# Kernel optimization log

Measured on AMD Instinct MI355X. Metric: run time of the kernel, lower is better.

The kernel has to match this reference:

```python
import jax, jax.numpy as jnp
import numpy as np

# Interpretation constants (external PersistentHomology class unavailable):
# each sample's feature vector is a point cloud of N_POINTS points in R^POINT_DIM.
N_POINTS = 1024
POINT_DIM = 128
WEIGHT = 1.0
N_TARGET_DIMS = 2  # target_dimensions = [0, 1]; H1 diagram is empty -> contributes 0


def _h0_mean_persistence(pts):
    """Exact H0 persistence of the Vietoris-Rips filtration of a point cloud.

    H0 pairs are (birth=0, death=w_e) for each edge w_e of the Euclidean MST,
    so persistence values are exactly the MST edge lengths (Prim's algorithm,
    vectorized over points, sequential over the N-1 tree-growth steps).
    pts: [N, d] -> scalar mean persistence.
    """
    n = pts.shape[0]
    mindist0 = jnp.linalg.norm(pts - pts[0], axis=-1)          # [N]
    visited0 = jnp.zeros((n,), dtype=bool).at[0].set(True)

    def step(carry, _):
        mindist, visited = carry
        masked = jnp.where(visited, jnp.inf, mindist)          # [N]
        j = jnp.argmin(masked)
        death = masked[j]                                      # MST edge length
        visited = visited.at[j].set(True)
        newd = jnp.linalg.norm(pts - pts[j], axis=-1)          # [N]
        mindist = jnp.minimum(mindist, newd)
        return (mindist, visited), death

    (_, _), deaths = jax.lax.scan(step, (mindist0, visited0), None, length=n - 1)
    return jnp.mean(deaths)


def setup_inputs() -> dict:
    key = jax.random.key(0)
    representations = jax.random.normal(key, (128, N_POINTS * POINT_DIM), dtype=jnp.float32)
    return {"representations": representations}


def reference(representations) -> jnp.ndarray:
    b = representations.shape[0]
    pts = representations.reshape(b, N_POINTS, POINT_DIM)      # per-sample point cloud
    per_sample = jax.vmap(_h0_mean_persistence)(pts)           # [B] mean H0 persistence
    # original: sum over batch and target dims (H1 empty), / (B * n_dims), * weight
    loss = jnp.sum(per_sample) / (b * N_TARGET_DIMS)
    return WEIGHT * loss
```

## Files before the change

kernel.cpp:

```cpp
#include <hip/hip_runtime.h>

typedef unsigned int uint_t;
typedef unsigned short ushort_t;
typedef unsigned char uchar_t;
typedef _Float16 h2 __attribute__((ext_vector_type(2)));
typedef _Float16 f16x8 __attribute__((ext_vector_type(8)));
typedef float f32x4 __attribute__((ext_vector_type(4)));

#define NPTS 1024
#define DIM  128
#define NH2  64

__device__ __forceinline__ float dot2f(uint_t a, uint_t b, float c) {
#if __has_builtin(__builtin_amdgcn_fdot2)
    return __builtin_amdgcn_fdot2(__builtin_bit_cast(h2, a),
                                  __builtin_bit_cast(h2, b), c, false);
#else
    h2 ha = __builtin_bit_cast(h2, a);
    h2 hb = __builtin_bit_cast(h2, b);
    c += (float)ha[0] * (float)hb[0];
    c += (float)ha[1] * (float)hb[1];
    return c;
#endif
}

__device__ __forceinline__ uint_t umin_u(uint_t a, uint_t b) { return a < b ? a : b; }
__device__ __forceinline__ uint_t umax_u(uint_t a, uint_t b) { return a > b ? a : b; }
__device__ __forceinline__ uint_t pk_min_u16(uint_t a, uint_t b) {
    uint_t d; asm("v_pk_min_u16 %0, %1, %2" : "=v"(d) : "v"(a), "v"(b)); return d;
}
__device__ __forceinline__ uint_t pk_max_u16(uint_t a, uint_t b) {
    uint_t d; asm("v_pk_max_u16 %0, %1, %2" : "=v"(d) : "v"(a), "v"(b)); return d;
}
__device__ __forceinline__ uint_t pk_sub_u16w(uint_t a, uint_t b) {
    uint_t d; asm("v_pk_sub_u16 %0, %1, %2" : "=v"(d) : "v"(a), "v"(b)); return d;
}

#define DPP_UMIN(x, ctrl)                                                       \
    x = umin_u(x, (uint_t)__builtin_amdgcn_update_dpp((int)(x), (int)(x),       \
                                                      (ctrl), 0xf, 0xf, false))
#define DPP_REDUCE(x)                                                           \
    do { DPP_UMIN(x, 0x111); DPP_UMIN(x, 0x112); DPP_UMIN(x, 0x114);            \
         DPP_UMIN(x, 0x118); DPP_UMIN(x, 0x142); DPP_UMIN(x, 0x143); } while (0)

#define SEL_LO 0x05020400u
#define SEL_HI 0x07020600u

__device__ __forceinline__ void gload16(const void* g, void* l) {
#if __has_builtin(__builtin_amdgcn_global_load_lds)
    __builtin_amdgcn_global_load_lds(
        (__attribute__((address_space(1))) void*)(g),
        (__attribute__((address_space(3))) void*)(l), 16, 0, 0);
#else
    *(uint4*)l = *(const uint4*)g;
#endif
}

__global__ __launch_bounds__(256)
void prep_kernel(const float* __restrict__ reps, ushort_t* __restrict__ P16,
                 float* __restrict__ norms) {
    const int t   = threadIdx.x;
    const int row = blockIdx.x * 16 + (t >> 4);
    const int kx  = (t & 15) * 8;
    const float* src = reps + (size_t)row * DIM + kx;
    float4 v0 = *(const float4*)src;
    float4 v1 = *(const float4*)(src + 4);
    _Float16 h[8] = {(_Float16)v0.x, (_Float16)v0.y, (_Float16)v0.z, (_Float16)v0.w,
                     (_Float16)v1.x, (_Float16)v1.y, (_Float16)v1.z, (_Float16)v1.w};
    float nrm = 0.f;
    uint_t pk[4];
#pragma unroll
    for (int i = 0; i < 4; ++i) {
        float a = (float)h[2 * i], b = (float)h[2 * i + 1];
        nrm += a * a + b * b;
        pk[i] = (uint_t)__builtin_bit_cast(ushort_t, h[2 * i]) |
                ((uint_t)__builtin_bit_cast(ushort_t, h[2 * i + 1]) << 16);
    }
    *(uint4*)(P16 + (size_t)row * DIM + kx) = make_uint4(pk[0], pk[1], pk[2], pk[3]);
#pragma unroll
    for (int m = 1; m <= 8; m <<= 1) nrm += __shfl_xor(nrm, m, 16);
    if ((t & 15) == 0) norms[row] = nrm;
}

__global__ __launch_bounds__(256)
void norms_kernel(const float* __restrict__ reps, float* __restrict__ norms) {
    const int t   = threadIdx.x;
    const int row = blockIdx.x * 16 + (t >> 4);
    const int kx  = (t & 15) * 8;
    const float* src = reps + (size_t)row * DIM + kx;
    float4 v0 = *(const float4*)src;
    float4 v1 = *(const float4*)(src + 4);
    float nrm = 0.f;
    {
        _Float16 h[8] = {(_Float16)v0.x, (_Float16)v0.y, (_Float16)v0.z, (_Float16)v0.w,
                         (_Float16)v1.x, (_Float16)v1.y, (_Float16)v1.z, (_Float16)v1.w};
#pragma unroll
        for (int i = 0; i < 8; ++i) { float a = (float)h[i]; nrm += a * a; }
    }
#pragma unroll
    for (int m = 1; m <= 8; m <<= 1) nrm += __shfl_xor(nrm, m, 16);
    if ((t & 15) == 0) norms[row] = nrm;
}

__device__ __forceinline__ int swz(int row, int seg) {
    return (row << 7) + (((seg ^ row) & 15) << 3);
}
__device__ __forceinline__ uint_t packh2(float a, float b) {
    h2 p; p[0] = (_Float16)a; p[1] = (_Float16)b;
    return __builtin_bit_cast(uint_t, p);
}

__device__ __forceinline__ void gram_core_epilogue(
        f32x4 acc[2][8], const float* nrmS, uchar_t* Ds,
        int ti, int tj, int lane, int w) {
    const int cj = lane & 15;
    const int r4 = (lane >> 4) * 4;
    float na[2][4], nb[8];
#pragma unroll
    for (int mt = 0; mt < 2; ++mt)
#pragma unroll
        for (int r = 0; r < 4; ++r)
            na[mt][r] = nrmS[ti * 128 + w * 32 + mt * 16 + r4 + r];
#pragma unroll
    for (int nt = 0; nt < 8; ++nt) nb[nt] = nrmS[tj * 128 + nt * 16 + cj];
#pragma unroll
    for (int mt = 0; mt < 2; ++mt)
#pragma unroll
        for (int nt = 0; nt < 8; ++nt) {
            const int gj = tj * 128 + nt * 16 + cj;
#pragma unroll
            for (int r = 0; r < 4; ++r) {
                const int gi = ti * 128 + w * 32 + mt * 16 + r4 + r;
                float d2 = fmaxf(na[mt][r] + nb[nt] - 2.f * acc[mt][nt][r], 0.f);
                uint_t q = (uint_t)(d2 * 0.5f + 0.5f);
                q = q > 255u ? 255u : q;
                Ds[((size_t)gi << 10) + gj] = (uchar_t)q;
            }
        }
}

__device__ __forceinline__ void stageB(const ushort_t* Ps, int tj,
                                       ushort_t* Bq, int t) {
#pragma unroll
    for (int i = 0; i < 8; ++i) {
        const int c   = t + i * 256;
        const int row = c >> 4;
        const int seg = (c ^ row) & 15;
        gload16(Ps + (((size_t)(tj * 128 + row)) << 7) + (size_t)seg * 8,
                Bq + (size_t)c * 8);
    }
}

__global__ __launch_bounds__(256, 2)
void gram16f_kernel(const ushort_t* __restrict__ P16, const float* __restrict__ norms,
                    uchar_t* __restrict__ D8, uint_t* __restrict__ NN4,
                    int xcd_affine) {
    __shared__ ushort_t Bt[2][128 * 128];
    __shared__ uchar_t  Ot[128 * 128];
    const int bid = blockIdx.x;
    int s, ti;
    if (xcd_affine) {
        const int x = bid & 7, k = bid >> 3;
        s  = x + ((k >> 3) << 3);
        ti = k & 7;
    } else {
        s  = bid >> 3;
        ti = bid & 7;
    }
    const int t = threadIdx.x, lane = t & 63, w = t >> 6;

    const ushort_t* Ps = P16 + ((size_t)s * NPTS << 7);
    const ushort_t* Pa = Ps + ((size_t)ti * 128 << 7);
    const float*  nrmS = norms + (size_t)s * NPTS;
    uchar_t*      Ds   = D8 + ((size_t)s << 20);

    const int mrow = lane & 15;
    const int lg   = lane >> 4;
    const int cj   = lane & 15;
    const int r4   = (lane >> 4) * 4;
    const uint_t rr  = (uint_t)(lane & 3);
    const uint_t cl4 = (uint_t)(lane & 12);

    float ha[2][4];
#pragma unroll
    for (int mt = 0; mt < 2; ++mt)
#pragma unroll
        for (int r = 0; r < 4; ++r)
            ha[mt][r] = 0.5f * nrmS[ti * 128 + w * 32 + mt * 16 + r4 + r] + 0.5f;

    const ushort_t* parow0 = Pa + ((w * 32 + mrow) << 7);
    const ushort_t* parow1 = Pa + ((w * 32 + 16 + mrow) << 7);

    uint_t nnr[2][4] = {{~0u, ~0u, ~0u, ~0u}, {~0u, ~0u, ~0u, ~0u}};

    const uint_t sel01 = rr | ((rr + 4u) << 8);

    stageB(Ps, 0, &Bt[0][0], t);
    __syncthreads();

    for (int tj = 0; tj < 8; ++tj) {
        ushort_t* Bq = &Bt[tj & 1][0];
        if (tj < 7) stageB(Ps, tj + 1, &Bt[(tj + 1) & 1][0], t);

        f32x4 acc[2][8] = {};
        f16x8 a0 = *(const f16x8*)(parow0 + lg * 8);
        f16x8 a1 = *(const f16x8*)(parow1 + lg * 8);
#pragma unroll
        for (int q = 0; q < 4; ++q) {
            const int seg = q * 4 + lg;
            f16x8 a0c = a0, a1c = a1;
            if (q < 3) {
                a0 = *(const f16x8*)(parow0 + ((q + 1) * 4 + lg) * 8);
                a1 = *(const f16x8*)(parow1 + ((q + 1) * 4 + lg) * 8);
            }
#pragma unroll
            for (int nt = 0; nt < 8; ++nt) {
                f16x8 b = *(const f16x8*)&Bq[swz(nt * 16 + mrow, seg)];
                acc[0][nt] = __builtin_amdgcn_mfma_f32_16x16x32_f16(a0c, b, acc[0][nt], 0, 0, 0);
                acc[1][nt] = __builtin_amdgcn_mfma_f32_16x16x32_f16(a1c, b, acc[1][nt], 0, 0, 0);
            }
        }

        float hb[8];
#pragma unroll
        for (int nt = 0; nt < 8; ++nt) hb[nt] = 0.5f * nrmS[tj * 128 + nt * 16 + cj];
        uint_t res[2][8];
#pragma unroll
        for (int mt = 0; mt < 2; ++mt)
#pragma unroll
            for (int nt = 0; nt < 8; ++nt) {
                uint_t cp = 0;
#pragma unroll
                for (int r = 0; r < 4; ++r) {
                    float f = (ha[mt][r] + hb[nt]) - acc[mt][nt][r];
#if __has_builtin(__builtin_amdgcn_cvt_pk_u8_f32)
                    cp = __builtin_amdgcn_cvt_pk_u8_f32(f, (uint_t)r, cp);
#else
                    uint_t qb = (uint_t)fminf(fmaxf(f, 0.f), 255.f);
                    cp |= qb << (8 * r);
#endif
                }
                uint_t d0 = (uint_t)__builtin_amdgcn_update_dpp((int)cp, (int)cp, 0x00, 0xf, 0xf, false);
                uint_t d1 = (uint_t)__builtin_amdgcn_update_dpp((int)cp, (int)cp, 0x55, 0xf, 0xf, false);
                uint_t d2 = (uint_t)__builtin_amdgcn_update_dpp((int)cp, (int)cp, 0xaa, 0xf, 0xf, false);
                uint_t d3 = (uint_t)__builtin_amdgcn_update_dpp((int)cp, (int)cp, 0xff, 0xf, 0xf, false);
                uint_t lo  = __builtin_amdgcn_perm(d1, d0, sel01);
                uint_t hi  = __builtin_amdgcn_perm(d3, d2, sel01);
                res[mt][nt] = __builtin_amdgcn_perm(hi, lo, 0x05040100u);
            }

        __syncthreads();
        const int lrb = w * 32 + r4 + (int)rr;
        const int c4b = lane & 12;
#pragma unroll
        for (int mt = 0; mt < 2; ++mt)
#pragma unroll
            for (int nt = 0; nt < 8; ++nt) {
                const int lr = lrb + mt * 16;
                const int cs = nt ^ (lr & 7);
                *(uint_t*)&Ot[lr * 128 + cs * 16 + c4b] = res[mt][nt];
            }
        __syncthreads();
        {
            const int r8 = lane >> 3, c = lane & 7;
#pragma unroll
            for (int k = 0; k < 4; ++k) {
                const int row = w * 32 + k * 8 + r8;
                const int cs  = c ^ (row & 7);
                uint4 vv = *(const uint4*)&Ot[row * 128 + cs * 16];
                *(uint4*)(Ds + (((size_t)(ti * 128 + row)) << 10) + tj * 128 + c * 16) = vv;
            }
        }

#pragma unroll
        for (int mt = 0; mt < 2; ++mt) {
            uint_t md[16];
#pragma unroll
            for (int nt = 0; nt < 8; ++nt) {
                const uint_t base = (uint_t)(nt * 16) + cl4;
                md[2 * nt]     = __builtin_amdgcn_perm(res[mt][nt],
                                     ((base + 1u) << 16) | base, SEL_LO);
                md[2 * nt + 1] = __builtin_amdgcn_perm(res[mt][nt],
                                     ((base + 3u) << 16) | (base + 2u), SEL_HI);
            }
            if (ti == tj) {
                const uint_t cs = (uint_t)(w * 32 + mt * 16 + r4) + rr;
#pragma unroll
                for (int m = 0; m < 16; ++m) {
                    const uint_t cb = (uint_t)((m >> 1) * 16) + cl4 + (uint_t)((m & 1) * 2);
                    uint_t h = (cs == cb) ? 0x0000FFFFu
                             : (cs == cb + 1u) ? 0xFFFF0000u : 0u;
                    md[m] |= h;
                }
            }
            uint_t prev = 0;
#pragma unroll
            for (int r = 0; r < 4; ++r) {
                uint_t tm[16];
                if (r == 0) {
#pragma unroll
                    for (int m = 0; m < 16; ++m) tm[m] = md[m];
                } else {
                    const uint_t dd = prev | (prev << 16);
#pragma unroll
                    for (int m = 0; m < 16; ++m) tm[m] = pk_sub_u16w(md[m], dd);
                }
                uint_t t0 = pk_min_u16(pk_min_u16(pk_min_u16(tm[0], tm[1]), pk_min_u16(tm[2], tm[3])),
                                       pk_min_u16(pk_min_u16(tm[4], tm[5]), pk_min_u16(tm[6], tm[7])));
                uint_t t1 = pk_min_u16(pk_min_u16(pk_min_u16(tm[8], tm[9]), pk_min_u16(tm[10], tm[11])),
                                       pk_min_u16(pk_min_u16(tm[12], tm[13]), pk_min_u16(tm[14], tm[15])));
                uint_t T = pk_min_u16(t0, t1);
                T = pk_min_u16(T, (uint_t)__builtin_amdgcn_ds_swizzle((int)T, 0x101F));
                T = pk_min_u16(T, (uint_t)__builtin_amdgcn_ds_swizzle((int)T, 0x201F));
                const uint_t v = umin_u(T & 0xFFFFu, T >> 16) + prev;
                prev = v + 1u;
                const uint_t g32 = ((v & 0xFF00u) << 2) | ((uint_t)tj << 7) | (v & 0x7Fu);
                uint_t x = g32, mm;
                mm = umin_u(nnr[mt][0], x); x = umax_u(nnr[mt][0], x); nnr[mt][0] = mm;
                mm = umin_u(nnr[mt][1], x); x = umax_u(nnr[mt][1], x); nnr[mt][1] = mm;
                mm = umin_u(nnr[mt][2], x); x = umax_u(nnr[mt][2], x); nnr[mt][2] = mm;
                nnr[mt][3] = umin_u(nnr[mt][3], x);
            }
        }
    }

    if ((lane & 12) == 0) {
#pragma unroll
        for (int mt = 0; mt < 2; ++mt) {
            const int grow = ti * 128 + w * 32 + mt * 16 + r4 + (int)rr;
            *(uint4*)(NN4 + ((size_t)s * NPTS + (size_t)grow) * 4) =
                make_uint4(nnr[mt][0], nnr[mt][1], nnr[mt][2], nnr[mt][3]);
        }
    }
}

__global__ __launch_bounds__(256, 2)
void gram_kernel(const float* __restrict__ reps, const float* __restrict__ norms,
                 uchar_t* __restrict__ D8, int s_base) {
    __shared__ ushort_t At[128 * 128];
    __shared__ ushort_t Bt[128 * 128];
    const int bid  = blockIdx.x;
    const int sl   = bid >> 6, tile = bid & 63, ti = tile >> 3, tj = tile & 7;
    const int s    = s_base + sl;
    const int t    = threadIdx.x, lane = t & 63, w = t >> 6;

    const float* Pa = reps + ((size_t)s * NPTS + (size_t)ti * 128) * DIM;
    const float* Pb = reps + ((size_t)s * NPTS + (size_t)tj * 128) * DIM;
#pragma unroll
    for (int i = 0; i < 8; ++i) {
        int c = t + i * 256, row = c >> 4, seg = c & 15;
        const float* pa = Pa + row * DIM + seg * 8;
        const float* pb = Pb + row * DIM + seg * 8;
        float4 a0 = *(const float4*)pa, a1 = *(const float4*)(pa + 4);
        float4 b0 = *(const float4*)pb, b1 = *(const float4*)(pb + 4);
        *(uint4*)&At[swz(row, seg)] = make_uint4(packh2(a0.x, a0.y), packh2(a0.z, a0.w),
                                                 packh2(a1.x, a1.y), packh2(a1.z, a1.w));
        *(uint4*)&Bt[swz(row, seg)] = make_uint4(packh2(b0.x, b0.y), packh2(b0.z, b0.w),
                                                 packh2(b1.x, b1.y), packh2(b1.z, b1.w));
    }
    __syncthreads();

    f32x4 acc[2][8] = {};
    const int mrow = lane & 15;
    const int lg   = lane >> 4;
#pragma unroll
    for (int q = 0; q < 4; ++q) {
        const int seg = q * 4 + lg;
        f16x8 a0 = *(const f16x8*)&At[swz(w * 32 + mrow, seg)];
        f16x8 a1 = *(const f16x8*)&At[swz(w * 32 + 16 + mrow, seg)];
#pragma unroll
        for (int nt = 0; nt < 8; ++nt) {
            f16x8 b = *(const f16x8*)&Bt[swz(nt * 16 + mrow, seg)];
            acc[0][nt] = __builtin_amdgcn_mfma_f32_16x16x32_f16(a0, b, acc[0][nt], 0, 0, 0);
            acc[1][nt] = __builtin_amdgcn_mfma_f32_16x16x32_f16(a1, b, acc[1][nt], 0, 0, 0);
        }
    }
    gram_core_epilogue(acc, norms + (size_t)s * NPTS, D8 + ((size_t)sl << 20),
                       ti, tj, lane, w);
}

__global__ __launch_bounds__(1024)
void boruvka4_kernel(const uchar_t* __restrict__ D8, const uint_t* __restrict__ NN4,
                     float* __restrict__ out, float scale) {
    const int sl   = blockIdx.x;
    const int v    = threadIdx.x;
    const int lane = v & 63;
    const int wv   = v >> 6;
    const uchar_t* Dbase = D8 + ((size_t)sl << 20);

    __shared__ ushort_t root16[NPTS];
    __shared__ uint_t   best[NPTS];
    __shared__ ushort_t rq[64];
    __shared__ uint_t   rqn, ncomp_s;
    __shared__ float    fsum[16];

    uint4 nA = *(const uint4*)(NN4 + (((size_t)sl << 10) + (size_t)v) * 4);
    uint_t nn[4] = {nA.x, nA.y, nA.z, nA.w};

    root16[v] = (ushort_t)v;
    float acc = 0.f;
    __syncthreads();

    for (int round = 0; round < 48; ++round) {
        best[v] = 0xFFFFFFFFu;
        if (v == 0) { rqn = 0; ncomp_s = 0; }
        __syncthreads();

        const uint_t rv = root16[v];

        uint_t cand = 0xFFFFFFFFu;
#pragma unroll
        for (int k = 0; k < 4; ++k) {
            uint_t e = nn[k];
            uint_t j = e & 1023u;
            if (root16[j] != (ushort_t)rv) {
                uint_t q = e >> 10;
                uint_t a = umin_u((uint_t)v, j), b = umax_u((uint_t)v, j);
                cand = umin_u(cand, (q << 20) | (a << 10) | b);
            }
        }
        if (cand != 0xFFFFFFFFu) atomicMin(&best[rv], cand);
        __syncthreads();

        if (rv == (uint_t)v && best[v] == 0xFFFFFFFFu) {
            uint_t idx = atomicAdd(&rqn, 1u);
            if (idx < 64u) rq[idx] = (ushort_t)v;
        }
        __syncthreads();

        if (rqn != 0u) {
            const uint_t nq = umin_u(rqn, 64u);
            for (uint_t qi = (uint_t)wv; qi < nq; qi += 16) {
                const uint_t row = rq[qi];
                const uint_t rr  = root16[row];
                uint4 r = ((const uint4*)(Dbase + ((size_t)row << 10)))[lane];
                uint_t bl = 0xFFFFFFFFu;
                const uint_t base = (uint_t)lane * 16u;
#pragma unroll
                for (int k = 0; k < 16; ++k) {
                    uint_t j = base + (uint_t)k;
                    uint_t q = (k < 4  ? (r.x >> (8 * k))
                              : k < 8  ? (r.y >> (8 * (k - 4)))
                              : k < 12 ? (r.z >> (8 * (k - 8)))
                                       : (r.w >> (8 * (k - 12)))) & 0xFFu;
                    uint_t a = umin_u(row, j), b = umax_u(row, j);
                    if (root16[j] != (ushort_t)rr)
                        bl = umin_u(bl, (q << 20) | (a << 10) | b);
                }
                DPP_REDUCE(bl);
                uint_t g = (uint_t)__builtin_amdgcn_readlane((int)bl, 63);
                if (lane == 0 && g != 0xFFFFFFFFu) atomicMin(&best[rr], g);
            }
            __syncthreads();
        }

        bool hook = false;
        uint_t o = (uint_t)v;
        if (rv == (uint_t)v) {
            uint_t K = best[v];
            if (K != 0xFFFFFFFFu) {
                uint_t a = (K >> 10) & 1023u, b = K & 1023u, q = K >> 20;
                uint_t ra = root16[a], rb = root16[b];
                o = (ra == (uint_t)v) ? rb : ra;
                if (o < (uint_t)v) {
                    hook = true;
                    acc += sqrtf(2.0f * (float)q);
                }
            }
        }
        __syncthreads();
        if (hook) root16[v] = (ushort_t)o;
        __syncthreads();

        uint_t r = root16[v];
        uint_t pr = root16[r];
        for (int sg = 0; sg < 64 && pr != r; ++sg) { r = pr; pr = root16[r]; }
        __syncthreads();
        root16[v] = (ushort_t)r;

        unsigned long long ball = __ballot(r == (uint_t)v);
        if (lane == 0) atomicAdd(&ncomp_s, (uint_t)__popcll(ball));
        __syncthreads();
        if (ncomp_s == 1u) break;
    }

#pragma unroll
    for (int m = 32; m >= 1; m >>= 1) acc += __shfl_xor(acc, m, 64);
    if (lane == 0) fsum[wv] = acc;
    __syncthreads();
    if (v == 0) {
        float s = 0.f;
#pragma unroll
        for (int i = 0; i < 16; ++i) s += fsum[i];
        atomicAdd(out, s * scale);
    }
}

__global__ __launch_bounds__(1024)
void boruvka_kernel(const uchar_t* __restrict__ D8, float* __restrict__ out,
                    float scale) {
    const int sl   = blockIdx.x;
    const int v    = threadIdx.x;
    const int lane = v & 63;
    const int wv   = v >> 6;
    const uchar_t* Dbase = D8 + ((size_t)sl << 20);

    __shared__ uint_t   nnlist[NPTS * 8];
    __shared__ ushort_t root16[NPTS];
    __shared__ uint_t   best[NPTS];
    __shared__ ushort_t rq[NPTS];
    __shared__ uint_t   rqn, ncomp_s;
    __shared__ float    fsum[16];

    uint_t slotv[8];
#pragma unroll
    for (int m = 0; m < 8; ++m)
        slotv[m] = ((uint_t)(2 * m + 1) << 16) | (uint_t)(2 * m);

    {
        uint4 rc = ((const uint4*)(Dbase + ((size_t)wv << 10)))[lane];
        for (int i = 0; i < 64; ++i) {
            const int row = wv + 16 * i;
            uint4 rn = rc;
            if (i < 63)
                rn = ((const uint4*)(Dbase + ((size_t)(row + 16) << 10)))[lane];
            uint_t md[8];
            md[0] = __builtin_amdgcn_perm(rc.x, slotv[0], SEL_LO);
            md[1] = __builtin_amdgcn_perm(rc.x, slotv[1], SEL_HI);
            md[2] = __builtin_amdgcn_perm(rc.y, slotv[2], SEL_LO);
            md[3] = __builtin_amdgcn_perm(rc.y, slotv[3], SEL_HI);
            md[4] = __builtin_amdgcn_perm(rc.z, slotv[4], SEL_LO);
            md[5] = __builtin_amdgcn_perm(rc.z, slotv[5], SEL_HI);
            md[6] = __builtin_amdgcn_perm(rc.w, slotv[6], SEL_LO);
            md[7] = __builtin_amdgcn_perm(rc.w, slotv[7], SEL_HI);
            {
                const bool win = (row >> 4) == lane;
                const uint_t s4 = (uint_t)(row & 15);
#pragma unroll
                for (int m = 0; m < 8; ++m) {
                    uint_t h = (win && s4 == 2u * m)      ? 0x0000FFFFu
                             : (win && s4 == 2u * m + 1u) ? 0xFFFF0000u : 0u;
                    md[m] |= h;
                }
            }
#pragma unroll
            for (int k = 0; k < 8; ++k) {
                uint_t t0 = pk_min_u16(pk_min_u16(md[0], md[1]), pk_min_u16(md[2], md[3]));
                uint_t t1 = pk_min_u16(pk_min_u16(md[4], md[5]), pk_min_u16(md[6], md[7]));
                uint_t tt = pk_min_u16(t0, t1);
                uint_t v16 = umin_u(tt & 0xFFFFu, tt >> 16);
                uint_t key = ((v16 & 0xFF00u) << 2) | ((uint_t)lane << 4) | (v16 & 15u);
                DPP_REDUCE(key);
                uint_t g = (uint_t)__builtin_amdgcn_readlane((int)key, 63);
                if (lane == 0) nnlist[row * 8 + k] = g;
                const uint_t wl = (g >> 4) & 63u, ws = g & 15u;
                const bool win = (uint_t)lane == wl;
#pragma unroll
                for (int m = 0; m < 8; ++m) {
                    uint_t h = (win && ws == 2u * m)      ? 0x0000FFFFu
                             : (win && ws == 2u * m + 1u) ? 0xFFFF0000u : 0u;
                    md[m] |= h;
                }
            }
            rc = rn;
        }
    }
    root16[v] = (ushort_t)v;
    __syncthreads();

    uint_t nn[8];
#pragma unroll
    for (int k = 0; k < 8; ++k) nn[k] = nnlist[v * 8 + k];
    const uint_t q8 = nn[7] >> 10;

    float acc = 0.f;
    for (int round = 0; round < 12; ++round) {
        best[v] = 0xFFFFFFFFu;
        if (v == 0) { rqn = 0; ncomp_s = 0; }
        __syncthreads();
        const uint_t rv = root16[v];
        uint_t cand = 0xFFFFFFFFu;
#pragma unroll
        for (int k = 0; k < 8; ++k) {
            uint_t e = nn[k];
            uint_t j = e & 1023u;
            if (root16[j] != (ushort_t)rv) {
                uint_t q = e >> 10;
                uint_t a = umin_u((uint_t)v, j), b = umax_u((uint_t)v, j);
                cand = umin_u(cand, (q << 20) | (a << 10) | b);
            }
        }
        if (cand != 0xFFFFFFFFu) atomicMin(&best[rv], cand);
        if (cand == 0xFFFFFFFFu || (cand >> 20) >= q8) {
            uint_t idx = atomicAdd(&rqn, 1u);
            rq[idx] = (ushort_t)v;
        }
        __syncthreads();
        for (uint_t qi = (uint_t)wv; qi < rqn; qi += 16) {
            const uint_t row = rq[qi];
            const uint_t rr  = root16[row];
            uint4 r = ((const uint4*)(Dbase + ((size_t)row << 10)))[lane];
            uint_t bl = 0xFFFFFFFFu;
            const uint_t base = (uint_t)lane * 16u;
#pragma unroll
            for (int k = 0; k < 16; ++k) {
                uint_t j = base + (uint_t)k;
                uint_t q = (k < 4  ? (r.x >> (8 * k))
                          : k < 8  ? (r.y >> (8 * (k - 4)))
                          : k < 12 ? (r.z >> (8 * (k - 8)))
                                   : (r.w >> (8 * (k - 12)))) & 0xFFu;
                uint_t a = umin_u(row, j), b = umax_u(row, j);
                if (root16[j] != (ushort_t)rr)
                    bl = umin_u(bl, (q << 20) | (a << 10) | b);
            }
            DPP_REDUCE(bl);
            uint_t g = (uint_t)__builtin_amdgcn_readlane((int)bl, 63);
            if (lane == 0 && g != 0xFFFFFFFFu) atomicMin(&best[rr], g);
        }
        __syncthreads();
        const bool isroot = (rv == (uint_t)v);
        bool hook = false;
        uint_t o = (uint_t)v;
        if (isroot) {
            uint_t K = best[v];
            if (K != 0xFFFFFFFFu) {
                uint_t a = (K >> 10) & 1023u, b = K & 1023u, q = K >> 20;
                uint_t ra = root16[a], rb = root16[b];
                o = (ra == (uint_t)v) ? rb : ra;
                bool mutual = (best[o] == K);
                if (!mutual || (uint_t)v > o) {
                    hook = true;
                    acc += sqrtf(2.0f * (float)q);
                }
            }
        }
        __syncthreads();
        if (hook) root16[v] = (ushort_t)o;
        __syncthreads();
        uint_t r = root16[v];
        uint_t pr = root16[r];
        for (int sgs = 0; sgs < 1024 && pr != r; ++sgs) { r = pr; pr = root16[r]; }
        __syncthreads();
        root16[v] = (ushort_t)r;
        unsigned long long ball = __ballot(r == (uint_t)v);
        if (lane == 0) atomicAdd(&ncomp_s, (uint_t)__popcll(ball));
        __syncthreads();
        if (ncomp_s == 1u) break;
    }
#pragma unroll
    for (int m = 32; m >= 1; m >>= 1) acc += __shfl_xor(acc, m, 64);
    if (lane == 0) fsum[wv] = acc;
    __syncthreads();
    if (v == 0) {
        float s = 0.f;
#pragma unroll
        for (int i = 0; i < 16; ++i) s += fsum[i];
        atomicAdd(out, s * scale);
    }
}

__global__ __launch_bounds__(64, 1)
void prim_u8_kernel(const uchar_t* __restrict__ D8, float* __restrict__ out,
                    float scale) {
    const int sl   = blockIdx.x;
    const int lane = threadIdx.x;
    const uchar_t* Dbase = D8 + ((size_t)sl << 20);

    uint_t md[8], po[8], slotv[8];
#pragma unroll
    for (int m = 0; m < 8; ++m) {
        md[m] = 0xFFFFFFFFu; po[m] = 0u;
        slotv[m] = ((uint_t)(2 * m + 1) << 16) | (uint_t)(2 * m);
    }
    const uint_t lane16 = (uint_t)lane << 4;
    uint_t p   = 0;
    float  acc = 0.f;

    for (int it = 0; it < NPTS - 1; ++it) {
        const uint4* rp = (const uint4*)(Dbase + ((size_t)p << 10));
        uint4 r = rp[lane];
        const bool  win = (p >> 4) == (uint_t)lane;
        const uint_t s4 = p & 15u;
#pragma unroll
        for (int m = 0; m < 8; ++m) {
            uint_t h = (win && s4 == 2u * m)      ? 0x0000FFFFu
                     : (win && s4 == 2u * m + 1u) ? 0xFFFF0000u : 0u;
            md[m] |= h; po[m] |= h;
        }
        md[0] = pk_min_u16(md[0], pk_max_u16(__builtin_amdgcn_perm(r.x, slotv[0], SEL_LO), po[0]));
        md[1] = pk_min_u16(md[1], pk_max_u16(__builtin_amdgcn_perm(r.x, slotv[1], SEL_HI), po[1]));
        md[2] = pk_min_u16(md[2], pk_max_u16(__builtin_amdgcn_perm(r.y, slotv[2], SEL_LO), po[2]));
        md[3] = pk_min_u16(md[3], pk_max_u16(__builtin_amdgcn_perm(r.y, slotv[3], SEL_HI), po[3]));
        md[4] = pk_min_u16(md[4], pk_max_u16(__builtin_amdgcn_perm(r.z, slotv[4], SEL_LO), po[4]));
        md[5] = pk_min_u16(md[5], pk_max_u16(__builtin_amdgcn_perm(r.z, slotv[5], SEL_HI), po[5]));
        md[6] = pk_min_u16(md[6], pk_max_u16(__builtin_amdgcn_perm(r.w, slotv[6], SEL_LO), po[6]));
        md[7] = pk_min_u16(md[7], pk_max_u16(__builtin_amdgcn_perm(r.w, slotv[7], SEL_HI), po[7]));

        uint_t t0 = pk_min_u16(pk_min_u16(md[0], md[1]), pk_min_u16(md[2], md[3]));
        uint_t t1 = pk_min_u16(pk_min_u16(md[4], md[5]), pk_min_u16(md[6], md[7]));
        uint_t tt = pk_min_u16(t0, t1);
        uint_t v16 = umin_u(tt & 0xFFFFu, tt >> 16);

        uint_t key = ((v16 & 0xFF00u) << 2) | lane16 | (v16 & 15u);
        DPP_REDUCE(key);
        uint_t g = (uint_t)__builtin_amdgcn_readlane((int)key, 63);

        p = g & 1023u;
        acc += sqrtf(2.0f * (float)(g >> 10));
    }
    if (lane == 0) atomicAdd(out, acc * scale);
}

#define NTHR 256
#define NWAVE 4
#define PPT  4
__global__ __launch_bounds__(NTHR, 1)
void prim_mst_kernel(const float* __restrict__ reps, float* __restrict__ out,
                     float scale) {
    const int s = blockIdx.x, t = threadIdx.x, lane = t & 63, wave = t >> 6;
    __shared__ uint4  sc[NH2 / 4];
    __shared__ float  snrm;
    __shared__ __align__(16) uint_t warr[NWAVE];
    __shared__ float  facc[NWAVE];
    uint_t cx[PPT][NH2]; float nrm[PPT], mind[PPT];
#pragma unroll
    for (int p = 0; p < PPT; ++p) {
        const float4* src = (const float4*)(reps + (size_t)s * (NPTS * DIM) +
                                            (size_t)(p * NTHR + t) * DIM);
        float n = 0.f;
#pragma unroll
        for (int k = 0; k < 32; ++k) {
            float4 v = src[k];
            h2 a; a[0] = (_Float16)v.x; a[1] = (_Float16)v.y;
            h2 b; b[0] = (_Float16)v.z; b[1] = (_Float16)v.w;
            cx[p][2 * k] = __builtin_bit_cast(uint_t, a);
            cx[p][2 * k + 1] = __builtin_bit_cast(uint_t, b);
            n = dot2f(cx[p][2 * k], cx[p][2 * k], n);
            n = dot2f(cx[p][2 * k + 1], cx[p][2 * k + 1], n);
        }
        nrm[p] = n; mind[p] = 3.0e38f;
    }
    uint_t vis = 0;
    if (t == 0) {
#pragma unroll
        for (int k = 0; k < NH2 / 4; ++k)
            sc[k] = make_uint4(cx[0][4 * k], cx[0][4 * k + 1], cx[0][4 * k + 2], cx[0][4 * k + 3]);
        snrm = nrm[0]; vis = 1;
    }
    __syncthreads();
    float acc = 0.f;
    for (int it = 0; it < NPTS - 1; ++it) {
        const float bn = snrm;
        float e0[PPT], e1[PPT];
#pragma unroll
        for (int p = 0; p < PPT; ++p) { e0[p] = 0.f; e1[p] = 0.f; }
#pragma unroll
        for (int k = 0; k < NH2 / 4; ++k) {
            uint4 q = sc[k];
#pragma unroll
            for (int p = 0; p < PPT; ++p) {
                e0[p] = dot2f(cx[p][4 * k + 0], q.x, e0[p]);
                e1[p] = dot2f(cx[p][4 * k + 1], q.y, e1[p]);
                e0[p] = dot2f(cx[p][4 * k + 2], q.z, e0[p]);
                e1[p] = dot2f(cx[p][4 * k + 3], q.w, e1[p]);
            }
        }
        uint_t key = 0xFFFFFFFFu;
#pragma unroll
        for (int p = 0; p < PPT; ++p) {
            float d2 = fmaxf(bn + nrm[p] - 2.f * (e0[p] + e1[p]), 0.f);
            mind[p] = fminf(mind[p], d2);
            uint_t kp = ((vis >> p) & 1u) ? 0xFFFFFFFFu
                      : ((__float_as_uint(mind[p]) & 0xFFFFFC00u) | (uint_t)(p * NTHR + t));
            key = umin_u(key, kp);
        }
        DPP_REDUCE(key);
        uint_t wkey = (uint_t)__builtin_amdgcn_readlane((int)key, 63);
        if (lane == 0) warr[wave] = wkey;
        __syncthreads();
        uint4 wv = *(const uint4*)warr;
        uint_t g = umin_u(umin_u(wv.x, wv.y), umin_u(wv.z, wv.w));
        const int j = (int)(g & 0x3FFu), jp = j >> 8;
        if ((j & (NTHR - 1)) == t) {
#pragma unroll
            for (int p = 0; p < PPT; ++p)
                if (jp == p) {
#pragma unroll
                    for (int k = 0; k < NH2 / 4; ++k)
                        sc[k] = make_uint4(cx[p][4 * k], cx[p][4 * k + 1],
                                           cx[p][4 * k + 2], cx[p][4 * k + 3]);
                    snrm = nrm[p]; acc += sqrtf(mind[p]);
                }
            vis |= 1u << jp;
        }
        __syncthreads();
    }
#pragma unroll
    for (int m = 32; m >= 1; m >>= 1) acc += __shfl_xor(acc, m, 64);
    if (lane == 0) facc[wave] = acc;
    __syncthreads();
    if (t == 0) atomicAdd(out, (facc[0] + facc[1] + facc[2] + facc[3]) * scale);
}

extern "C" void kernel_launch(void* const* d_in, const int* in_sizes, int n_in,
                              void* d_out, int out_size, void* d_ws, size_t ws_size,
                              hipStream_t stream) {
    const float* reps = (const float*)d_in[0];
    float*       out  = (float*)d_out;
    const int ns = in_sizes[0] / (NPTS * DIM);
    const float scale = 1.0f / ((float)(NPTS - 1) * (float)ns * 2.0f);

    hipMemsetAsync(out, 0, sizeof(float), stream);

    const size_t bytes_D  = (size_t)ns << 20;
    const size_t bytes_P  = (size_t)ns << 18;
    const size_t bytes_NN = (size_t)ns << 14;
    const size_t bytes_N  = (size_t)ns << 12;

    if (ws_size >= bytes_D + bytes_P + bytes_NN + bytes_N) {
        uchar_t*  D8    = (uchar_t*)d_ws;
        ushort_t* P16   = (ushort_t*)((char*)d_ws + bytes_D);
        uint_t*   NN4   = (uint_t*)((char*)d_ws + bytes_D + bytes_P);
        float*    norms = (float*)((char*)d_ws + bytes_D + bytes_P + bytes_NN);
        const int xcd_affine = ((ns & 7) == 0) ? 1 : 0;
        prep_kernel<<<dim3(ns * 64), dim3(256), 0, stream>>>(reps, P16, norms);
        gram16f_kernel<<<dim3(ns * 8), dim3(256), 0, stream>>>(P16, norms, D8, NN4,
                                                               xcd_affine);
        boruvka4_kernel<<<dim3(ns), dim3(1024), 0, stream>>>(D8, NN4, out, scale);
    } else if (ws_size >= bytes_D + bytes_N) {
        uchar_t* D8    = (uchar_t*)d_ws;
        float*   norms = (float*)((char*)d_ws + bytes_D);
        norms_kernel<<<dim3(ns * 64), dim3(256), 0, stream>>>(reps, norms);
        gram_kernel<<<dim3(ns * 64), dim3(256), 0, stream>>>(reps, norms, D8, 0);
        boruvka_kernel<<<dim3(ns), dim3(1024), 0, stream>>>(D8, out, scale);
    } else {
        int nc = 0;
        size_t norms_off = 0;
        if (ws_size > bytes_N + (1u << 20)) {
            norms_off = (ws_size - bytes_N) & ~(size_t)15;
            nc = (int)(norms_off >> 20);
            if (nc > ns) nc = ns;
        }
        if (nc >= 32) {
            uchar_t* D8    = (uchar_t*)d_ws;
            float*   norms = (float*)((char*)d_ws + norms_off);
            norms_kernel<<<dim3(ns * 64), dim3(256), 0, stream>>>(reps, norms);
            for (int base = 0; base < ns; base += nc) {
                const int n = (ns - base < nc) ? (ns - base) : nc;
                gram_kernel<<<dim3(n * 64), dim3(256), 0, stream>>>(reps, norms, D8, base);
                prim_u8_kernel<<<dim3(n), dim3(64), 0, stream>>>(D8, out, scale);
            }
        } else {
            prim_mst_kernel<<<dim3(ns), dim3(NTHR), 0, stream>>>(reps, out, scale);
        }
    }
}
```

Baseline: 210.5 us.

## Shrink gram tile to 64 rows to double block count and occupancy

The fused fp16 Gram + per-row nearest-neighbour kernel now handles 64-row strips with 64-column tiles instead of 128x128. Each wave handles 16 rows, launch bounds go from 2 to 4 blocks per CU, and the grid doubles to ns*16 blocks. The goal is better CU fill on the 256-CU part, since 1024 blocks at 2 per CU left occupancy low, and better latency hiding. The cost is that each loaded B tile is reused half as much, so L2 and LDS traffic rise, and the top-4 packing changes its column-index bit layout.

Result: slower. 228.4 us (+8.5%).

```diff
diff --git a/kernel.cpp b/kernel.cpp
--- a/kernel.cpp
+++ b/kernel.cpp
@@ -139,38 +139,38 @@
         }
 }
 
-__device__ __forceinline__ void stageB(const ushort_t* Ps, int tj,
-                                       ushort_t* Bq, int t) {
-#pragma unroll
-    for (int i = 0; i < 8; ++i) {
+__device__ __forceinline__ void stageB64(const ushort_t* Ps, int tj,
+                                         ushort_t* Bq, int t) {
+#pragma unroll
+    for (int i = 0; i < 4; ++i) {
         const int c   = t + i * 256;
         const int row = c >> 4;
         const int seg = (c ^ row) & 15;
-        gload16(Ps + (((size_t)(tj * 128 + row)) << 7) + (size_t)seg * 8,
+        gload16(Ps + (((size_t)(tj * 64 + row)) << 7) + (size_t)seg * 8,
                 Bq + (size_t)c * 8);
     }
 }
 
-__global__ __launch_bounds__(256, 2)
+__global__ __launch_bounds__(256, 4)
 void gram16f_kernel(const ushort_t* __restrict__ P16, const float* __restrict__ norms,
                     uchar_t* __restrict__ D8, uint_t* __restrict__ NN4,
                     int xcd_affine) {
-    __shared__ ushort_t Bt[2][128 * 128];
-    __shared__ uchar_t  Ot[128 * 128];
+    __shared__ ushort_t Bt[2][64 * 128];
+    __shared__ uchar_t  Ot[64 * 64];
     const int bid = blockIdx.x;
     int s, ti;
     if (xcd_affine) {
         const int x = bid & 7, k = bid >> 3;
-        s  = x + ((k >> 3) << 3);
-        ti = k & 7;
+        s  = x + ((k >> 4) << 3);
+        ti = k & 15;
     } else {
-        s  = bid >> 3;
-        ti = bid & 7;
+        s  = bid >> 4;
+        ti = bid & 15;
     }
     const int t = threadIdx.x, lane = t & 63, w = t >> 6;
 
     const ushort_t* Ps = P16 + ((size_t)s * NPTS << 7);
-    const ushort_t* Pa = Ps + ((size_t)ti * 128 << 7);
+    const ushort_t* Pa = Ps + ((size_t)ti * 64 << 7);
     const float*  nrmS = norms + (size_t)s * NPTS;
     uchar_t*      Ds   = D8 + ((size_t)s << 20);
 
@@ -181,112 +181,95 @@
     const uint_t rr  = (uint_t)(lane & 3);
     const uint_t cl4 = (uint_t)(lane & 12);
 
-    float ha[2][4];
-#pragma unroll
-    for (int mt = 0; mt < 2; ++mt)
-#pragma unroll
-        for (int r = 0; r < 4; ++r)
-            ha[mt][r] = 0.5f * nrmS[ti * 128 + w * 32 + mt * 16 + r4 + r] + 0.5f;
-
-    const ushort_t* parow0 = Pa + ((w * 32 + mrow) << 7);
-    const ushort_t* parow1 = Pa + ((w * 32 + 16 + mrow) << 7);
-
-    uint_t nnr[2][4] = {{~0u, ~0u, ~0u, ~0u}, {~0u, ~0u, ~0u, ~0u}};
+    float ha[4];
+#pragma unroll
+    for (int r = 0; r < 4; ++r)
+        ha[r] = 0.5f * nrmS[ti * 64 + w * 16 + r4 + r] + 0.5f;
+
+    const ushort_t* parow0 = Pa + ((w * 16 + mrow) << 7);
+
+    uint_t nnr[4] = {~0u, ~0u, ~0u, ~0u};
 
     const uint_t sel01 = rr | ((rr + 4u) << 8);
 
-    stageB(Ps, 0, &Bt[0][0], t);
+    stageB64(Ps, 0, &Bt[0][0], t);
     __syncthreads();
 
-    for (int tj = 0; tj < 8; ++tj) {
+    for (int tj = 0; tj < 16; ++tj) {
         ushort_t* Bq = &Bt[tj & 1][0];
-        if (tj < 7) stageB(Ps, tj + 1, &Bt[(tj + 1) & 1][0], t);
-
-        f32x4 acc[2][8] = {};
+        if (tj < 15) stageB64(Ps, tj + 1, &Bt[(tj + 1) & 1][0], t);
+
+        f32x4 acc[4] = {};
         f16x8 a0 = *(const f16x8*)(parow0 + lg * 8);
-        f16x8 a1 = *(const f16x8*)(parow1 + lg * 8);
 #pragma unroll
         for (int q = 0; q < 4; ++q) {
             const int seg = q * 4 + lg;
-            f16x8 a0c = a0, a1c = a1;
-            if (q < 3) {
-                a0 = *(const f16x8*)(parow0 + ((q + 1) * 4 + lg) * 8);
-                a1 = *(const f16x8*)(parow1 + ((q + 1) * 4 + lg) * 8);
-            }
-#pragma unroll
-            for (int nt = 0; nt < 8; ++nt) {
+            f16x8 a0c = a0;
+            if (q < 3) a0 = *(const f16x8*)(parow0 + ((q + 1) * 4 + lg) * 8);
+#pragma unroll
+            for (int nt = 0; nt < 4; ++nt) {
                 f16x8 b = *(const f16x8*)&Bq[swz(nt * 16 + mrow, seg)];
-                acc[0][nt] = __builtin_amdgcn_mfma_f32_16x16x32_f16(a0c, b, acc[0][nt], 0, 0, 0);
-                acc[1][nt] = __builtin_amdgcn_mfma_f32_16x16x32_f16(a1c, b, acc[1][nt], 0, 0, 0);
-            }
-        }
-
-        float hb[8];
-#pragma unroll
-        for (int nt = 0; nt < 8; ++nt) hb[nt] = 0.5f * nrmS[tj * 128 + nt * 16 + cj];
-        uint_t res[2][8];
-#pragma unroll
-        for (int mt = 0; mt < 2; ++mt)
-#pragma unroll
-            for (int nt = 0; nt < 8; ++nt) {
-                uint_t cp = 0;
-#pragma unroll
-                for (int r = 0; r < 4; ++r) {
-                    float f = (ha[mt][r] + hb[nt]) - acc[mt][nt][r];
+                acc[nt] = __builtin_amdgcn_mfma_f32_16x16x32_f16(a0c, b, acc[nt], 0, 0, 0);
+            }
+        }
+
+        float hb[4];
+#pragma unroll
+        for (int nt = 0; nt < 4; ++nt) hb[nt] = 0.5f * nrmS[tj * 64 + nt * 16 + cj];
+        uint_t res[4];
+#pragma unroll
+        for (int nt = 0; nt < 4; ++nt) {
+            uint_t cp = 0;
+#pragma unroll
+            for (int r = 0; r < 4; ++r) {
+                float f = (ha[r] + hb[nt]) - acc[nt][r];
 #if __has_builtin(__builtin_amdgcn_cvt_pk_u8_f32)
-                    cp = __builtin_amdgcn_cvt_pk_u8_f32(f, (uint_t)r, cp);
+                cp = __builtin_amdgcn_cvt_pk_u8_f32(f, (uint_t)r, cp);
 #else
-                    uint_t qb = (uint_t)fminf(fmaxf(f, 0.f), 255.f);
-                    cp |= qb << (8 * r);
+                uint_t qb = (uint_t)fminf(fmaxf(f, 0.f), 255.f);
+                cp |= qb << (8 * r);
 #endif
-                }
-                uint_t d0 = (uint_t)__builtin_amdgcn_update_dpp((int)cp, (int)cp, 0x00, 0xf, 0xf, false);
-                uint_t d1 = (uint_t)__builtin_amdgcn_update_dpp((int)cp, (int)cp, 0x55, 0xf, 0xf, false);
-                uint_t d2 = (uint_t)__builtin_amdgcn_update_dpp((int)cp, (int)cp, 0xaa, 0xf, 0xf, false);
-                uint_t d3 = (uint_t)__builtin_amdgcn_update_dpp((int)cp, (int)cp, 0xff, 0xf, 0xf, false);
-                uint_t lo  = __builtin_amdgcn_perm(d1, d0, sel01);
-                uint_t hi  = __builtin_amdgcn_perm(d3, d2, sel01);
-                res[mt][nt] = __builtin_amdgcn_perm(hi, lo, 0x05040100u);
-            }
-
-        __syncthreads();
-        const int lrb = w * 32 + r4 + (int)rr;
+            }
+            uint_t d0 = (uint_t)__builtin_amdgcn_update_dpp((int)cp, (int)cp, 0x00, 0xf, 0xf, false);
+            uint_t d1 = (uint_t)__builtin_amdgcn_update_dpp((int)cp, (int)cp, 0x55, 0xf, 0xf, false);
+            uint_t d2 = (uint_t)__builtin_amdgcn_update_dpp((int)cp, (int)cp, 0xaa, 0xf, 0xf, false);
+            uint_t d3 = (uint_t)__builtin_amdgcn_update_dpp((int)cp, (int)cp, 0xff, 0xf, 0xf, false);
+            uint_t lo  = __builtin_amdgcn_perm(d1, d0, sel01);
+            uint_t hi  = __builtin_amdgcn_perm(d3, d2, sel01);
+            res[nt] = __builtin_amdgcn_perm(hi, lo, 0x05040100u);
+        }
+
+        __syncthreads();
+        const int lr  = w * 16 + r4 + (int)rr;
         const int c4b = lane & 12;
 #pragma unroll
-        for (int mt = 0; mt < 2; ++mt)
-#pragma unroll
-            for (int nt = 0; nt < 8; ++nt) {
-                const int lr = lrb + mt * 16;
-                const int cs = nt ^ (lr & 7);
-                *(uint_t*)&Ot[lr * 128 + cs * 16 + c4b] = res[mt][nt];
-            }
+        for (int nt = 0; nt < 4; ++nt) {
+            const int cs = nt ^ (lr & 3);
+            *(uint_t*)&Ot[lr * 64 + cs * 16 + c4b] = res[nt];
+        }
         __syncthreads();
         {
-            const int r8 = lane >> 3, c = lane & 7;
-#pragma unroll
-            for (int k = 0; k < 4; ++k) {
-                const int row = w * 32 + k * 8 + r8;
-                const int cs  = c ^ (row & 7);
-                uint4 vv = *(const uint4*)&Ot[row * 128 + cs * 16];
-                *(uint4*)(Ds + (((size_t)(ti * 128 + row)) << 10) + tj * 128 + c * 16) = vv;
-            }
-        }
-
-#pragma unroll
-        for (int mt = 0; mt < 2; ++mt) {
-            uint_t md[16];
-#pragma unroll
-            for (int nt = 0; nt < 8; ++nt) {
+            const int r8 = lane >> 2, c = lane & 3;
+            const int row = w * 16 + r8;
+            const int cs  = c ^ (row & 3);
+            uint4 vv = *(const uint4*)&Ot[row * 64 + cs * 16];
+            *(uint4*)(Ds + (((size_t)(ti * 64 + row)) << 10) + tj * 64 + c * 16) = vv;
+        }
+
+        {
+            uint_t md[8];
+#pragma unroll
+            for (int nt = 0; nt < 4; ++nt) {
                 const uint_t base = (uint_t)(nt * 16) + cl4;
-                md[2 * nt]     = __builtin_amdgcn_perm(res[mt][nt],
+                md[2 * nt]     = __builtin_amdgcn_perm(res[nt],
                                      ((base + 1u) << 16) | base, SEL_LO);
-                md[2 * nt + 1] = __builtin_amdgcn_perm(res[mt][nt],
+                md[2 * nt + 1] = __builtin_amdgcn_perm(res[nt],
                                      ((base + 3u) << 16) | (base + 2u), SEL_HI);
             }
             if (ti == tj) {
-                const uint_t cs = (uint_t)(w * 32 + mt * 16 + r4) + rr;
-#pragma unroll
-                for (int m = 0; m < 16; ++m) {
+                const uint_t cs = (uint_t)(w * 16 + r4) + rr;
+#pragma unroll
+                for (int m = 0; m < 8; ++m) {
                     const uint_t cb = (uint_t)((m >> 1) * 16) + cl4 + (uint_t)((m & 1) * 2);
                     uint_t h = (cs == cb) ? 0x0000FFFFu
                              : (cs == cb + 1u) ? 0xFFFF0000u : 0u;
@@ -296,41 +279,36 @@
             uint_t prev = 0;
 #pragma unroll
             for (int r = 0; r < 4; ++r) {
-                uint_t tm[16];
+                uint_t tm[8];
                 if (r == 0) {
 #pragma unroll
-                    for (int m = 0; m < 16; ++m) tm[m] = md[m];
+                    for (int m = 0; m < 8; ++m) tm[m] = md[m];
                 } else {
                     const uint_t dd = prev | (prev << 16);
 #pragma unroll
-                    for (int m = 0; m < 16; ++m) tm[m] = pk_sub_u16w(md[m], dd);
+                    for (int m = 0; m < 8; ++m) tm[m] = pk_sub_u16w(md[m], dd);
                 }
-                uint_t t0 = pk_min_u16(pk_min_u16(pk_min_u16(tm[0], tm[1]), pk_min_u16(tm[2], tm[3])),
-                                       pk_min_u16(pk_min_u16(tm[4], tm[5]), pk_min_u16(tm[6], tm[7])));
-                uint_t t1 = pk_min_u16(pk_min_u16(pk_min_u16(tm[8], tm[9]), pk_min_u16(tm[10], tm[11])),
-                                       pk_min_u16(pk_min_u16(tm[12], tm[13]), pk_min_u16(tm[14], tm[15])));
+                uint_t t0 = pk_min_u16(pk_min_u16(tm[0], tm[1]), pk_min_u16(tm[2], tm[3]));
+                uint_t t1 = pk_min_u16(pk_min_u16(tm[4], tm[5]), pk_min_u16(tm[6], tm[7]));
                 uint_t T = pk_min_u16(t0, t1);
                 T = pk_min_u16(T, (uint_t)__builtin_amdgcn_ds_swizzle((int)T, 0x101F));
                 T = pk_min_u16(T, (uint_t)__builtin_amdgcn_ds_swizzle((int)T, 0x201F));
                 const uint_t v = umin_u(T & 0xFFFFu, T >> 16) + prev;
                 prev = v + 1u;
-                const uint_t g32 = ((v & 0xFF00u) << 2) | ((uint_t)tj << 7) | (v & 0x7Fu);
+                const uint_t g32 = ((v & 0xFF00u) << 2) | ((uint_t)tj << 6) | (v & 0x3Fu);
                 uint_t x = g32, mm;
-                mm = umin_u(nnr[mt][0], x); x = umax_u(nnr[mt][0], x); nnr[mt][0] = mm;
-                mm = umin_u(nnr[mt][1], x); x = umax_u(nnr[mt][1], x); nnr[mt][1] = mm;
-                mm = umin_u(nnr[mt][2], x); x = umax_u(nnr[mt][2], x); nnr[mt][2] = mm;
-                nnr[mt][3] = umin_u(nnr[mt][3], x);
+                mm = umin_u(nnr[0], x); x = umax_u(nnr[0], x); nnr[0] = mm;
+                mm = umin_u(nnr[1], x); x = umax_u(nnr[1], x); nnr[1] = mm;
+                mm = umin_u(nnr[2], x); x = umax_u(nnr[2], x); nnr[2] = mm;
+                nnr[3] = umin_u(nnr[3], x);
             }
         }
     }
 
     if ((lane & 12) == 0) {
-#pragma unroll
-        for (int mt = 0; mt < 2; ++mt) {
-            const int grow = ti * 128 + w * 32 + mt * 16 + r4 + (int)rr;
-            *(uint4*)(NN4 + ((size_t)s * NPTS + (size_t)grow) * 4) =
-                make_uint4(nnr[mt][0], nnr[mt][1], nnr[mt][2], nnr[mt][3]);
-        }
+        const int grow = ti * 64 + w * 16 + r4 + (int)rr;
+        *(uint4*)(NN4 + ((size_t)s * NPTS + (size_t)grow) * 4) =
+            make_uint4(nnr[0], nnr[1], nnr[2], nnr[3]);
     }
 }
 
@@ -824,8 +802,8 @@
         float*    norms = (float*)((char*)d_ws + bytes_D + bytes_P + bytes_NN);
         const int xcd_affine = ((ns & 7) == 0) ? 1 : 0;
         prep_kernel<<<dim3(ns * 64), dim3(256), 0, stream>>>(reps, P16, norms);
-        gram16f_kernel<<<dim3(ns * 8), dim3(256), 0, stream>>>(P16, norms, D8, NN4,
-                                                               xcd_affine);
+        gram16f_kernel<<<dim3(ns * 16), dim3(256), 0, stream>>>(P16, norms, D8, NN4,
+                                                                xcd_affine);
         boruvka4_kernel<<<dim3(ns), dim3(1024), 0, stream>>>(D8, NN4, out, scale);
     } else if (ws_size >= bytes_D + bytes_N) {
         uchar_t* D8    = (uchar_t*)d_ws;
```
